# Performance work log

Measured on AMD Instinct MI355X. Metric: run time of the kernel, lower is better.

The kernel has to match this reference:

```python
import jax, jax.numpy as jnp
import numpy as np

B, D, H, DEPTH = 1024, 1024, 1024, 4


def setup_inputs() -> dict:
    key = jax.random.key(0)
    k_x, k_w, k_ws, k_bs = jax.random.split(key, 4)
    x = jax.random.normal(k_x, (B, D), dtype=jnp.float32)
    W_enc = jax.random.normal(k_w, (D, H), dtype=jnp.float32) * 0.02
    b_enc = jnp.zeros((H,), dtype=jnp.float32)
    # per-layer CrossNet weights, matching keras random_normal init (stddev=0.05)
    ws = jax.random.normal(k_ws, (DEPTH, H, 1), dtype=jnp.float32) * 0.05
    bs = jax.random.normal(k_bs, (DEPTH, H, 1), dtype=jnp.float32) * 0.05
    return {"x": x, "W_enc": W_enc, "b_enc": b_enc, "ws": ws, "bs": bs}


def reference(x, W_enc, b_enc, ws, bs):
    # encoder Dense
    h = jnp.matmul(x, W_enc) + b_enc  # (B, H)
    x0 = h
    x_l = h
    depth = ws.shape[0]
    for l in range(depth):
        # original: (x0[:, :, None] * x_l[:, None, :]) @ w + b, squeezed.
        # outer[b,i,j] @ w  == x0[b,i] * sum_j x_l[b,j] * w[j]
        s = jnp.matmul(x_l, ws[l])            # (B, 1)
        residual = x0 * s + bs[l][:, 0]       # (B, H)
        x_l = residual + x_l
    return x_l
```

## Files before the change

### kernel.cpp

```cpp
#include <hip/hip_runtime.h>
#include <hip/hip_bf16.h>


#define B_SZ 1024
#define D_SZ 1024
#define H_SZ 1024
#define DEPTH 4

typedef _Float16 half4_t __attribute__((ext_vector_type(4)));
typedef _Float16 half8_t __attribute__((ext_vector_type(8)));
typedef float floatx4_t __attribute__((ext_vector_type(4)));

typedef const __attribute__((address_space(1))) unsigned int* gas_ptr;
typedef __attribute__((address_space(3))) unsigned int* las_ptr;

__device__ __forceinline__ void async_copy16(const void* g, void* l) {
    __builtin_amdgcn_global_load_lds((gas_ptr)g, (las_ptr)l, 16, 0, 0);
}

__global__ __launch_bounds__(256) void prep_kernel(
        const float* __restrict__ x, const float* __restrict__ W,
        _Float16* __restrict__ xh, _Float16* __restrict__ Wt) {
    const int b = blockIdx.x;
    const int t = threadIdx.x;
    if (b < 256) {
        __shared__ float S[64][65];
        const int k0 = (b >> 4) << 6;
        const int n0 = (b & 15) << 6;
#pragma unroll
        for (int i = 0; i < 4; ++i) {
            int idx = (i << 8) + t;
            int r = idx >> 4;
            int c4 = idx & 15;
            float4 v = *(const float4*)(W + (size_t)(k0 + r) * H_SZ + n0 + (c4 << 2));
            S[r][(c4 << 2) + 0] = v.x;
            S[r][(c4 << 2) + 1] = v.y;
            S[r][(c4 << 2) + 2] = v.z;
            S[r][(c4 << 2) + 3] = v.w;
        }
        __syncthreads();
#pragma unroll
        for (int i = 0; i < 4; ++i) {
            int idx = (i << 8) + t;
            int n = idx >> 4;
            int c4 = idx & 15;
            int k = c4 << 2;
            half4_t o;
            o.x = (_Float16)S[k + 0][n];
            o.y = (_Float16)S[k + 1][n];
            o.z = (_Float16)S[k + 2][n];
            o.w = (_Float16)S[k + 3][n];
            *(half4_t*)(Wt + (size_t)(n0 + n) * D_SZ + k0 + k) = o;
        }
    } else {
        const int base = (b - 256) * 4096;
#pragma unroll
        for (int i = 0; i < 4; ++i) {
            int off = base + (((i << 8) + t) << 2);
            float4 v = *(const float4*)(x + off);
            half4_t o;
            o.x = (_Float16)v.x; o.y = (_Float16)v.y;
            o.z = (_Float16)v.z; o.w = (_Float16)v.w;
            *(half4_t*)(xh + off) = o;
        }
    }
}

__global__ __launch_bounds__(512) void gemm_kernel(
        const _Float16* __restrict__ xh, const _Float16* __restrict__ Wt,
        float* __restrict__ h) {
    __shared__ _Float16 As[2][32 * 64];
    __shared__ _Float16 Bs[2][64 * 64];
    const int tid  = threadIdx.x;
    const int lane = tid & 63;
    const int w    = tid >> 6;
    const int m0 = blockIdx.y << 5;
    const int n0 = blockIdx.x << 6;
    const int wm = (w >> 2) << 4;
    const int wn = (w & 3) << 4;

    const int sr = tid >> 3;
    const int sc = ((tid & 7) ^ (sr & 7)) << 3;
    const _Float16* aSrc = xh + (size_t)(m0 + (sr & 31)) * D_SZ + sc;
    const _Float16* bSrc = Wt + (size_t)(n0 + sr) * D_SZ + sc;

    const int ra = wm + (lane & 15);
    const int rb = wn + (lane & 15);
    const int q  = lane >> 4;

    floatx4_t acc = {0.0f, 0.0f, 0.0f, 0.0f};

    if (tid < 256) async_copy16(aSrc, &As[0][tid << 3]);
    async_copy16(bSrc, &Bs[0][tid << 3]);

    for (int it = 0; it < 16; ++it) {
        __syncthreads();
        if (it + 1 < 16) {
            int k0 = (it + 1) << 6;
            int buf = (it + 1) & 1;
            if (tid < 256) async_copy16(aSrc + k0, &As[buf][tid << 3]);
            async_copy16(bSrc + k0, &Bs[buf][tid << 3]);
        }
        const _Float16* Ab = As[it & 1];
        const _Float16* Bb = Bs[it & 1];
#pragma unroll
        for (int kk = 0; kk < 2; ++kk) {
            int l = (kk << 2) + q;
            half8_t af = *(const half8_t*)(Ab + ra * 64 + ((l ^ (ra & 7)) << 3));
            half8_t bf = *(const half8_t*)(Bb + rb * 64 + ((l ^ (rb & 7)) << 3));
            acc = __builtin_amdgcn_mfma_f32_16x16x32_f16(af, bf, acc, 0, 0, 0);
        }
    }

    const int col = n0 + wn + (lane & 15);
    const int row0 = m0 + wm + (q << 2);
#pragma unroll
    for (int r = 0; r < 4; ++r)
        h[(size_t)(row0 + r) * H_SZ + col] = acc[r];
}

__global__ __launch_bounds__(256) void crossnet_kernel(
        float* __restrict__ h, const float* __restrict__ b_enc,
        const float* __restrict__ ws, const float* __restrict__ bs) {
    const int row = blockIdx.x;
    const int t = threadIdx.x;
    float* hr = h + (size_t)row * H_SZ;

    float4 hv = *(const float4*)(hr + (t << 2));
    float4 be = *(const float4*)(b_enc + (t << 2));
    float4 wv[DEPTH], bv[DEPTH];
#pragma unroll
    for (int l = 0; l < DEPTH; ++l) {
        wv[l] = *(const float4*)(ws + l * H_SZ + (t << 2));
        bv[l] = *(const float4*)(bs + l * H_SZ + (t << 2));
    }
    float x0[4] = {hv.x + be.x, hv.y + be.y, hv.z + be.z, hv.w + be.w};
    float xl[4] = {x0[0], x0[1], x0[2], x0[3]};

    __shared__ float red[DEPTH][4];

#pragma unroll
    for (int l = 0; l < DEPTH; ++l) {
        float p = xl[0] * wv[l].x + xl[1] * wv[l].y + xl[2] * wv[l].z + xl[3] * wv[l].w;
#pragma unroll
        for (int off = 32; off > 0; off >>= 1) p += __shfl_down(p, off, 64);
        if ((t & 63) == 0) red[l][t >> 6] = p;
        __syncthreads();
        float s = red[l][0] + red[l][1] + red[l][2] + red[l][3];
        xl[0] += x0[0] * s + bv[l].x;
        xl[1] += x0[1] * s + bv[l].y;
        xl[2] += x0[2] * s + bv[l].z;
        xl[3] += x0[3] * s + bv[l].w;
    }
    float4 o = {xl[0], xl[1], xl[2], xl[3]};
    *(float4*)(hr + (t << 2)) = o;
}

extern "C" void kernel_launch(void* const* d_in, const int* in_sizes, int n_in,
                              void* d_out, int out_size, void* d_ws, size_t ws_size,
                              hipStream_t stream) {
    const float* x     = (const float*)d_in[0];
    const float* W_enc = (const float*)d_in[1];
    const float* b_enc = (const float*)d_in[2];
    const float* ws    = (const float*)d_in[3];
    const float* bs    = (const float*)d_in[4];
    float* out = (float*)d_out;

    _Float16* xh = (_Float16*)d_ws;
    _Float16* Wt = xh + (size_t)B_SZ * D_SZ;

    prep_kernel<<<512, 256, 0, stream>>>(x, W_enc, xh, Wt);
    dim3 grid(H_SZ / 64, B_SZ / 32);
    gemm_kernel<<<grid, 512, 0, stream>>>(xh, Wt, out);
    crossnet_kernel<<<B_SZ, 256, 0, stream>>>(out, b_enc, ws, bs);
}
```

Baseline: 82.34 us.

## Collapse CrossNet recurrence algebraically and enlarge GEMM tiles to 64x64x128

The CrossNet layers are rewritten in closed form. Each x_l is expressed as x0*sig plus a cumulative bias sum, so the four dependent block reductions become a single batched reduction of x0·w_l. The weight-only scalars (cumulative bias dot w_l, and the summed bias vector) are computed once in an extra prep block. Separately, the GEMM tile grows to 64x64 with K-step 128 and two MFMA accumulators per wave, which halves the block count and the number of K iterations but uses more LDS per block.

```diff
diff --git a/kernel.cpp b/kernel.cpp
--- a/kernel.cpp
+++ b/kernel.cpp
@@ -1,5 +1,4 @@
 #include <hip/hip_runtime.h>
-#include <hip/hip_bf16.h>
 
 
 #define B_SZ 1024
@@ -20,7 +19,9 @@
 
 __global__ __launch_bounds__(256) void prep_kernel(
         const float* __restrict__ x, const float* __restrict__ W,
-        _Float16* __restrict__ xh, _Float16* __restrict__ Wt) {
+        const float* __restrict__ ws, const float* __restrict__ bs,
+        _Float16* __restrict__ xh, _Float16* __restrict__ Wt,
+        float* __restrict__ cvec, float* __restrict__ beta4) {
     const int b = blockIdx.x;
     const int t = threadIdx.x;
     if (b < 256) {
@@ -52,7 +53,7 @@
             o.w = (_Float16)S[k + 3][n];
             *(half4_t*)(Wt + (size_t)(n0 + n) * D_SZ + k0 + k) = o;
         }
-    } else {
+    } else if (b < 512) {
         const int base = (b - 256) * 4096;
 #pragma unroll
         for (int i = 0; i < 4; ++i) {
@@ -63,97 +64,153 @@
             o.z = (_Float16)v.z; o.w = (_Float16)v.w;
             *(half4_t*)(xh + off) = o;
         }
-    }
-}
-
-__global__ __launch_bounds__(512) void gemm_kernel(
+    } else {
+        __shared__ float redc[4][3];
+        const int j = t << 2;
+        float4 b0 = *(const float4*)(bs + 0 * H_SZ + j);
+        float4 b1 = *(const float4*)(bs + 1 * H_SZ + j);
+        float4 b2 = *(const float4*)(bs + 2 * H_SZ + j);
+        float4 b3 = *(const float4*)(bs + 3 * H_SZ + j);
+        float4 w1 = *(const float4*)(ws + 1 * H_SZ + j);
+        float4 w2 = *(const float4*)(ws + 2 * H_SZ + j);
+        float4 w3 = *(const float4*)(ws + 3 * H_SZ + j);
+        float4 pre1 = b0;
+        float4 pre2 = {pre1.x + b1.x, pre1.y + b1.y, pre1.z + b1.z, pre1.w + b1.w};
+        float4 pre3 = {pre2.x + b2.x, pre2.y + b2.y, pre2.z + b2.z, pre2.w + b2.w};
+        float4 bt   = {pre3.x + b3.x, pre3.y + b3.y, pre3.z + b3.z, pre3.w + b3.w};
+        *(float4*)(beta4 + j) = bt;
+        float pp[3];
+        pp[0] = pre1.x * w1.x + pre1.y * w1.y + pre1.z * w1.z + pre1.w * w1.w;
+        pp[1] = pre2.x * w2.x + pre2.y * w2.y + pre2.z * w2.z + pre2.w * w2.w;
+        pp[2] = pre3.x * w3.x + pre3.y * w3.y + pre3.z * w3.z + pre3.w * w3.w;
+#pragma unroll
+        for (int off = 32; off > 0; off >>= 1) {
+#pragma unroll
+            for (int l = 0; l < 3; ++l) pp[l] += __shfl_down(pp[l], off, 64);
+        }
+        if ((t & 63) == 0) {
+#pragma unroll
+            for (int l = 0; l < 3; ++l) redc[t >> 6][l] = pp[l];
+        }
+        __syncthreads();
+        if (t == 0) {
+            cvec[0] = 0.0f;
+#pragma unroll
+            for (int l = 0; l < 3; ++l)
+                cvec[l + 1] = redc[0][l] + redc[1][l] + redc[2][l] + redc[3][l];
+        }
+    }
+}
+
+__global__ __launch_bounds__(512, 2) void gemm_kernel(
         const _Float16* __restrict__ xh, const _Float16* __restrict__ Wt,
         float* __restrict__ h) {
-    __shared__ _Float16 As[2][32 * 64];
-    __shared__ _Float16 Bs[2][64 * 64];
+    __shared__ _Float16 As[2][64 * 128];
+    __shared__ _Float16 Bs[2][64 * 128];
     const int tid  = threadIdx.x;
     const int lane = tid & 63;
     const int w    = tid >> 6;
-    const int m0 = blockIdx.y << 5;
+    const int m0 = blockIdx.y << 6;
     const int n0 = blockIdx.x << 6;
-    const int wm = (w >> 2) << 4;
+    const int wm = (w >> 2) << 5;
     const int wn = (w & 3) << 4;
 
-    const int sr = tid >> 3;
-    const int sc = ((tid & 7) ^ (sr & 7)) << 3;
-    const _Float16* aSrc = xh + (size_t)(m0 + (sr & 31)) * D_SZ + sc;
-    const _Float16* bSrc = Wt + (size_t)(n0 + sr) * D_SZ + sc;
+    const int r0 = tid >> 4;
+    const int c0 = ((tid & 15) ^ (r0 & 15)) << 3;
+    const int r1 = r0 + 32;
+    const int c1 = ((tid & 15) ^ (r1 & 15)) << 3;
+    const _Float16* aSrc0 = xh + (size_t)(m0 + r0) * D_SZ + c0;
+    const _Float16* aSrc1 = xh + (size_t)(m0 + r1) * D_SZ + c1;
+    const _Float16* bSrc0 = Wt + (size_t)(n0 + r0) * D_SZ + c0;
+    const _Float16* bSrc1 = Wt + (size_t)(n0 + r1) * D_SZ + c1;
 
     const int ra = wm + (lane & 15);
     const int rb = wn + (lane & 15);
     const int q  = lane >> 4;
 
-    floatx4_t acc = {0.0f, 0.0f, 0.0f, 0.0f};
-
-    if (tid < 256) async_copy16(aSrc, &As[0][tid << 3]);
-    async_copy16(bSrc, &Bs[0][tid << 3]);
-
-    for (int it = 0; it < 16; ++it) {
+    floatx4_t acc0 = {0.0f, 0.0f, 0.0f, 0.0f};
+    floatx4_t acc1 = {0.0f, 0.0f, 0.0f, 0.0f};
+
+    async_copy16(aSrc0, &As[0][tid << 3]);
+    async_copy16(aSrc1, &As[0][(tid + 512) << 3]);
+    async_copy16(bSrc0, &Bs[0][tid << 3]);
+    async_copy16(bSrc1, &Bs[0][(tid + 512) << 3]);
+
+    for (int it = 0; it < 8; ++it) {
         __syncthreads();
-        if (it + 1 < 16) {
-            int k0 = (it + 1) << 6;
+        if (it + 1 < 8) {
+            int k0 = (it + 1) << 7;
             int buf = (it + 1) & 1;
-            if (tid < 256) async_copy16(aSrc + k0, &As[buf][tid << 3]);
-            async_copy16(bSrc + k0, &Bs[buf][tid << 3]);
+            async_copy16(aSrc0 + k0, &As[buf][tid << 3]);
+            async_copy16(aSrc1 + k0, &As[buf][(tid + 512) << 3]);
+            async_copy16(bSrc0 + k0, &Bs[buf][tid << 3]);
+            async_copy16(bSrc1 + k0, &Bs[buf][(tid + 512) << 3]);
         }
         const _Float16* Ab = As[it & 1];
         const _Float16* Bb = Bs[it & 1];
 #pragma unroll
-        for (int kk = 0; kk < 2; ++kk) {
+        for (int kk = 0; kk < 4; ++kk) {
             int l = (kk << 2) + q;
-            half8_t af = *(const half8_t*)(Ab + ra * 64 + ((l ^ (ra & 7)) << 3));
-            half8_t bf = *(const half8_t*)(Bb + rb * 64 + ((l ^ (rb & 7)) << 3));
-            acc = __builtin_amdgcn_mfma_f32_16x16x32_f16(af, bf, acc, 0, 0, 0);
-        }
-    }
-
-    const int col = n0 + wn + (lane & 15);
+            int swz = (l ^ (ra & 15)) << 3;
+            half8_t bf = *(const half8_t*)(Bb + rb * 128 + ((l ^ (rb & 15)) << 3));
+            half8_t a0 = *(const half8_t*)(Ab + ra * 128 + swz);
+            half8_t a1 = *(const half8_t*)(Ab + (ra + 16) * 128 + swz);
+            acc0 = __builtin_amdgcn_mfma_f32_16x16x32_f16(a0, bf, acc0, 0, 0, 0);
+            acc1 = __builtin_amdgcn_mfma_f32_16x16x32_f16(a1, bf, acc1, 0, 0, 0);
+        }
+    }
+
+    const int col  = n0 + wn + (lane & 15);
     const int row0 = m0 + wm + (q << 2);
 #pragma unroll
-    for (int r = 0; r < 4; ++r)
-        h[(size_t)(row0 + r) * H_SZ + col] = acc[r];
+    for (int r = 0; r < 4; ++r) {
+        h[(size_t)(row0 + r) * H_SZ + col] = acc0[r];
+        h[(size_t)(row0 + 16 + r) * H_SZ + col] = acc1[r];
+    }
 }
 
 __global__ __launch_bounds__(256) void crossnet_kernel(
         float* __restrict__ h, const float* __restrict__ b_enc,
-        const float* __restrict__ ws, const float* __restrict__ bs) {
+        const float* __restrict__ ws, const float* __restrict__ cvec,
+        const float* __restrict__ beta4) {
     const int row = blockIdx.x;
     const int t = threadIdx.x;
+    const int j = t << 2;
     float* hr = h + (size_t)row * H_SZ;
 
-    float4 hv = *(const float4*)(hr + (t << 2));
-    float4 be = *(const float4*)(b_enc + (t << 2));
-    float4 wv[DEPTH], bv[DEPTH];
+    float4 hv = *(const float4*)(hr + j);
+    float4 be = *(const float4*)(b_enc + j);
+    float x0[4] = {hv.x + be.x, hv.y + be.y, hv.z + be.z, hv.w + be.w};
+
+    float p[DEPTH];
 #pragma unroll
     for (int l = 0; l < DEPTH; ++l) {
-        wv[l] = *(const float4*)(ws + l * H_SZ + (t << 2));
-        bv[l] = *(const float4*)(bs + l * H_SZ + (t << 2));
-    }
-    float x0[4] = {hv.x + be.x, hv.y + be.y, hv.z + be.z, hv.w + be.w};
-    float xl[4] = {x0[0], x0[1], x0[2], x0[3]};
-
-    __shared__ float red[DEPTH][4];
-
+        float4 wv = *(const float4*)(ws + l * H_SZ + j);
+        p[l] = x0[0] * wv.x + x0[1] * wv.y + x0[2] * wv.z + x0[3] * wv.w;
+    }
+#pragma unroll
+    for (int off = 32; off > 0; off >>= 1) {
+#pragma unroll
+        for (int l = 0; l < DEPTH; ++l) p[l] += __shfl_down(p[l], off, 64);
+    }
+    __shared__ float red[4][DEPTH];
+    if ((t & 63) == 0) {
+#pragma unroll
+        for (int l = 0; l < DEPTH; ++l) red[t >> 6][l] = p[l];
+    }
+    __syncthreads();
+
+    float sig = 1.0f;
 #pragma unroll
     for (int l = 0; l < DEPTH; ++l) {
-        float p = xl[0] * wv[l].x + xl[1] * wv[l].y + xl[2] * wv[l].z + xl[3] * wv[l].w;
-#pragma unroll
-        for (int off = 32; off > 0; off >>= 1) p += __shfl_down(p, off, 64);
-        if ((t & 63) == 0) red[l][t >> 6] = p;
-        __syncthreads();
-        float s = red[l][0] + red[l][1] + red[l][2] + red[l][3];
-        xl[0] += x0[0] * s + bv[l].x;
-        xl[1] += x0[1] * s + bv[l].y;
-        xl[2] += x0[2] * s + bv[l].z;
-        xl[3] += x0[3] * s + bv[l].w;
-    }
-    float4 o = {xl[0], xl[1], xl[2], xl[3]};
-    *(float4*)(hr + (t << 2)) = o;
+        float d = red[0][l] + red[1][l] + red[2][l] + red[3][l];
+        float s = sig * d + cvec[l];
+        sig += s;
+    }
+    float4 b4 = *(const float4*)(beta4 + j);
+    float4 o = {x0[0] * sig + b4.x, x0[1] * sig + b4.y,
+                x0[2] * sig + b4.z, x0[3] * sig + b4.w};
+    *(float4*)(hr + j) = o;
 }
 
 extern "C" void kernel_launch(void* const* d_in, const int* in_sizes, int n_in,
@@ -168,9 +225,12 @@
 
     _Float16* xh = (_Float16*)d_ws;
     _Float16* Wt = xh + (size_t)B_SZ * D_SZ;
-
-    prep_kernel<<<512, 256, 0, stream>>>(x, W_enc, xh, Wt);
-    dim3 grid(H_SZ / 64, B_SZ / 32);
+    float* aux   = (float*)((char*)d_ws + 4u * 1024u * 1024u);
+    float* cvec  = aux;
+    float* beta4 = aux + 4;
+
+    prep_kernel<<<513, 256, 0, stream>>>(x, W_enc, ws, bs, xh, Wt, cvec, beta4);
+    dim3 grid(H_SZ / 64, B_SZ / 64);
     gemm_kernel<<<grid, 512, 0, stream>>>(xh, Wt, out);
-    crossnet_kernel<<<B_SZ, 256, 0, stream>>>(out, b_enc, ws, bs);
-}
+    crossnet_kernel<<<B_SZ, 256, 0, stream>>>(out, b_enc, ws, cvec, beta4);
+}
```

New measurement: 80.81 us. Within noise of the previous version (-1.9%).
